# Performance work log

Hardware: AMD Instinct MI355X
Metric: run time of the kernel (lower is better)

Reference implementation:

```python
import jax, jax.numpy as jnp
import numpy as np
from jax import lax

EPS = 1e-08

def _sobel_edges(x, sx, sy):
    # x: [B, C, H, W]; depthwise 3x3 conv per channel, SAME padding.
    B, C, H, W = x.shape
    kx = jnp.tile(sx, (C, 1, 1, 1))  # [C,1,3,3] OIHW with feature_group_count=C
    ky = jnp.tile(sy, (C, 1, 1, 1))
    dn = ('NCHW', 'OIHW', 'NCHW')
    gx = lax.conv_general_dilated(x, kx, (1, 1), 'SAME',
                                  dimension_numbers=dn, feature_group_count=C)
    gy = lax.conv_general_dilated(x, ky, (1, 1), 'SAME',
                                  dimension_numbers=dn, feature_group_count=C)
    return jnp.sqrt(gx * gx + gy * gy + EPS)

def setup_inputs() -> dict:
    key = jax.random.key(0)
    k1, k2 = jax.random.split(key)
    B, C, H, W = 16, 8, 512, 512
    source_latent = jax.random.normal(k1, (B, C, H, W), dtype=jnp.float32)
    edited_latent = jax.random.normal(k2, (B, C, H, W), dtype=jnp.float32)
    sx = jnp.array([[-1., 0., 1.], [-2., 0., 2.], [-1., 0., 1.]], dtype=jnp.float32).reshape(1, 1, 3, 3)
    sy = jnp.array([[-1., -2., -1.], [0., 0., 0.], [1., 2., 1.]], dtype=jnp.float32).reshape(1, 1, 3, 3)
    return {"source_latent": source_latent, "edited_latent": edited_latent, "sx": sx, "sy": sy}

def reference(source_latent, edited_latent, sx, sy):
    e_src = _sobel_edges(source_latent, sx, sy)
    e_edit = _sobel_edges(edited_latent, sx, sy)
    diff = e_edit - e_src
    return jnp.mean(diff * diff)
```

## Files before the change

kernel.cpp:

```cpp
#include <hip/hip_runtime.h>


#define EPS 1e-8f

constexpr int W_DIM  = 512;
constexpr int H_DIM  = 512;
constexpr int NIMG   = 128;
constexpr int ROWS   = 16;
constexpr int CHUNKS = H_DIM / ROWS;
constexpr int TPB    = 128;
constexpr int NBLK   = NIMG * CHUNKS;
constexpr double TOTAL_ELEMS = 33554432.0;

__global__ __launch_bounds__(TPB) void edge_loss_stage1(
    const float* __restrict__ src, const float* __restrict__ edt,
    float* __restrict__ partial)
{
    const int blk   = blockIdx.x;
    const int n     = blk / CHUNKS;
    const int chunk = blk % CHUNKS;
    const int r0    = chunk * ROWS;
    const float* sbase = src + (size_t)n * H_DIM * W_DIM;
    const float* ebase = edt + (size_t)n * H_DIM * W_DIM;
    const int c0 = threadIdx.x * 4;

    float sa0[4], sa1[4], sa2[4], sb0[4], sb1[4], sb2[4];
    float ea0[4], ea1[4], ea2[4], eb0[4], eb1[4], eb2[4];

    auto loadrow = [&](const float* base, int h, float* a, float* b) {
        if (h < 0 || h >= H_DIM) {
            #pragma unroll
            for (int i = 0; i < 4; ++i) { a[i] = 0.f; b[i] = 0.f; }
            return;
        }
        const float* row = base + (size_t)h * W_DIM;
        float4 v = *reinterpret_cast<const float4*>(row + c0);
        float xl = (c0 > 0)          ? row[c0 - 1] : 0.f;
        float xr = (c0 + 4 < W_DIM)  ? row[c0 + 4] : 0.f;
        float p0 = xl,  p1 = v.x, p2 = v.y, p3 = v.z, p4 = v.w, p5 = xr;
        a[0] = p2 - p0;  b[0] = p0 + 2.f*p1 + p2;
        a[1] = p3 - p1;  b[1] = p1 + 2.f*p2 + p3;
        a[2] = p4 - p2;  b[2] = p2 + 2.f*p3 + p4;
        a[3] = p5 - p3;  b[3] = p3 + 2.f*p4 + p5;
    };

    loadrow(sbase, r0 - 1, sa0, sb0);
    loadrow(ebase, r0 - 1, ea0, eb0);
    loadrow(sbase, r0,     sa1, sb1);
    loadrow(ebase, r0,     ea1, eb1);

    float acc = 0.f;
    for (int h = r0; h < r0 + ROWS; ++h) {
        loadrow(sbase, h + 1, sa2, sb2);
        loadrow(ebase, h + 1, ea2, eb2);
        #pragma unroll
        for (int i = 0; i < 4; ++i) {
            float sgx = sa0[i] + 2.f*sa1[i] + sa2[i];
            float sgy = sb2[i] - sb0[i];
            float es  = __builtin_amdgcn_sqrtf(sgx*sgx + sgy*sgy + EPS);
            float egx = ea0[i] + 2.f*ea1[i] + ea2[i];
            float egy = eb2[i] - eb0[i];
            float ee  = __builtin_amdgcn_sqrtf(egx*egx + egy*egy + EPS);
            float d   = ee - es;
            acc += d * d;
        }
        #pragma unroll
        for (int i = 0; i < 4; ++i) {
            sa0[i] = sa1[i]; sa1[i] = sa2[i];
            sb0[i] = sb1[i]; sb1[i] = sb2[i];
            ea0[i] = ea1[i]; ea1[i] = ea2[i];
            eb0[i] = eb1[i]; eb1[i] = eb2[i];
        }
    }

    #pragma unroll
    for (int off = 32; off > 0; off >>= 1)
        acc += __shfl_down(acc, off);
    __shared__ float wsum[TPB / 64];
    const int wid  = threadIdx.x >> 6;
    const int lane = threadIdx.x & 63;
    if (lane == 0) wsum[wid] = acc;
    __syncthreads();
    if (threadIdx.x == 0) {
        float tot = 0.f;
        #pragma unroll
        for (int i = 0; i < TPB / 64; ++i) tot += wsum[i];
        partial[blk] = tot;
    }
}

__global__ __launch_bounds__(256) void edge_loss_stage2(
    const float* __restrict__ partial, float* __restrict__ out, int nparts)
{
    double acc = 0.0;
    for (int i = threadIdx.x; i < nparts; i += 256)
        acc += (double)partial[i];
    #pragma unroll
    for (int off = 32; off > 0; off >>= 1)
        acc += __shfl_down(acc, off);
    __shared__ double wsum[4];
    const int wid  = threadIdx.x >> 6;
    const int lane = threadIdx.x & 63;
    if (lane == 0) wsum[wid] = acc;
    __syncthreads();
    if (threadIdx.x == 0) {
        double t = 0.0;
        #pragma unroll
        for (int i = 0; i < 4; ++i) t += wsum[i];
        out[0] = (float)(t / TOTAL_ELEMS);
    }
}

extern "C" void kernel_launch(void* const* d_in, const int* in_sizes, int n_in,
                              void* d_out, int out_size, void* d_ws, size_t ws_size,
                              hipStream_t stream) {
    const float* src = (const float*)d_in[0];
    const float* edt = (const float*)d_in[1];
    float* out     = (float*)d_out;
    float* partial = (float*)d_ws;

    edge_loss_stage1<<<dim3(NBLK), dim3(TPB), 0, stream>>>(src, edt, partial);
    edge_loss_stage2<<<dim3(1), dim3(256), 0, stream>>>(partial, out, NBLK);
}
```

Before: 57.23 us.

## Use one wavefront per 512-wide row with 8 columns per lane and shuffled halos

Each wavefront now covers a full 512-wide row, with every lane holding 8 contiguous columns. Halo columns come from cross-lane shuffles rather than extra scalar global loads. Rows are double-buffered so the load for the next row is issued before the current row is consumed, and the vertical Sobel sums are carried as running partial accumulators. Blocks grow to 4 waves covering 64 rows each. This removes the redundant halo loads, raises the load width, and overlaps memory latency with compute, at the cost of more registers per thread.

New measurement: 123.1 us. +115.0%, slower.

```diff
diff --git a/kernel.cpp b/kernel.cpp
--- a/kernel.cpp
+++ b/kernel.cpp
@@ -3,88 +3,161 @@
 
 #define EPS 1e-8f
 
-constexpr int W_DIM  = 512;
-constexpr int H_DIM  = 512;
-constexpr int NIMG   = 128;
-constexpr int ROWS   = 16;
-constexpr int CHUNKS = H_DIM / ROWS;
-constexpr int TPB    = 128;
-constexpr int NBLK   = NIMG * CHUNKS;
+constexpr int W_DIM = 512;
+constexpr int H_DIM = 512;
+constexpr int NIMG  = 128;
+constexpr int ROWS  = 16;
+constexpr int WPB   = 4;
+constexpr int TPB   = 64 * WPB;
+constexpr int BLK_ROWS = ROWS * WPB;
+constexpr int BLKS_PER_IMG = H_DIM / BLK_ROWS;
+constexpr int NBLK  = NIMG * BLKS_PER_IMG;
 constexpr double TOTAL_ELEMS = 33554432.0;
 
-__global__ __launch_bounds__(TPB) void edge_loss_stage1(
+__global__ __launch_bounds__(TPB, 4) void edge_loss_stage1(
     const float* __restrict__ src, const float* __restrict__ edt,
     float* __restrict__ partial)
 {
-    const int blk   = blockIdx.x;
-    const int n     = blk / CHUNKS;
-    const int chunk = blk % CHUNKS;
-    const int r0    = chunk * ROWS;
-    const float* sbase = src + (size_t)n * H_DIM * W_DIM;
-    const float* ebase = edt + (size_t)n * H_DIM * W_DIM;
-    const int c0 = threadIdx.x * 4;
+    const int blk  = blockIdx.x;
+    const int img  = blk / BLKS_PER_IMG;
+    const int brow = (blk % BLKS_PER_IMG) * BLK_ROWS;
+    const int wid  = threadIdx.x >> 6;
+    const int lane = threadIdx.x & 63;
+    const int r0   = brow + wid * ROWS;
+    const int c0   = lane * 8;
 
-    float sa0[4], sa1[4], sa2[4], sb0[4], sb1[4], sb2[4];
-    float ea0[4], ea1[4], ea2[4], eb0[4], eb1[4], eb2[4];
+    const float* sbase = src + (size_t)img * (H_DIM * W_DIM) + c0;
+    const float* ebase = edt + (size_t)img * (H_DIM * W_DIM) + c0;
 
-    auto loadrow = [&](const float* base, int h, float* a, float* b) {
-        if (h < 0 || h >= H_DIM) {
-            #pragma unroll
-            for (int i = 0; i < 4; ++i) { a[i] = 0.f; b[i] = 0.f; }
-            return;
-        }
-        const float* row = base + (size_t)h * W_DIM;
-        float4 v = *reinterpret_cast<const float4*>(row + c0);
-        float xl = (c0 > 0)          ? row[c0 - 1] : 0.f;
-        float xr = (c0 + 4 < W_DIM)  ? row[c0 + 4] : 0.f;
-        float p0 = xl,  p1 = v.x, p2 = v.y, p3 = v.z, p4 = v.w, p5 = xr;
-        a[0] = p2 - p0;  b[0] = p0 + 2.f*p1 + p2;
-        a[1] = p3 - p1;  b[1] = p1 + 2.f*p2 + p3;
-        a[2] = p4 - p2;  b[2] = p2 + 2.f*p3 + p4;
-        a[3] = p5 - p3;  b[3] = p3 + 2.f*p4 + p5;
+    float sP0[8], sP1[8], sB0[8], sB1[8];
+    float eP0[8], eP1[8], eB0[8], eB1[8];
+    float spA[8], epA[8], spB[8], epB[8];
+    float acc = 0.f;
+
+    auto issue = [&](int h, float* sp, float* ep) {
+        int hc = h < 0 ? 0 : (h >= H_DIM ? H_DIM - 1 : h);
+        const float* srow = sbase + (size_t)hc * W_DIM;
+        const float* erow = ebase + (size_t)hc * W_DIM;
+        float4 s0 = reinterpret_cast<const float4*>(srow)[0];
+        float4 s1 = reinterpret_cast<const float4*>(srow)[1];
+        float4 e0 = reinterpret_cast<const float4*>(erow)[0];
+        float4 e1 = reinterpret_cast<const float4*>(erow)[1];
+        sp[0]=s0.x; sp[1]=s0.y; sp[2]=s0.z; sp[3]=s0.w;
+        sp[4]=s1.x; sp[5]=s1.y; sp[6]=s1.z; sp[7]=s1.w;
+        ep[0]=e0.x; ep[1]=e0.y; ep[2]=e0.z; ep[3]=e0.w;
+        ep[4]=e1.x; ep[5]=e1.y; ep[6]=e1.z; ep[7]=e1.w;
     };
 
-    loadrow(sbase, r0 - 1, sa0, sb0);
-    loadrow(ebase, r0 - 1, ea0, eb0);
-    loadrow(sbase, r0,     sa1, sb1);
-    loadrow(ebase, r0,     ea1, eb1);
+    auto consume = [&](const float* sp, const float* ep, int h) {
+        if (h < H_DIM) {
+            float spL = __shfl_up(sp[7], 1);  spL = lane ? spL : 0.f;
+            float spR = __shfl_down(sp[0], 1); spR = (lane == 63) ? 0.f : spR;
+            float epL = __shfl_up(ep[7], 1);  epL = lane ? epL : 0.f;
+            float epR = __shfl_down(ep[0], 1); epR = (lane == 63) ? 0.f : epR;
+            #pragma unroll
+            for (int i = 0; i < 8; ++i) {
+                float sm = (i == 0) ? spL : sp[i-1];
+                float sq = (i == 7) ? spR : sp[i+1];
+                float a  = sq - sm;
+                float b  = sm + 2.f*sp[i] + sq;
+                float gx = sP0[i] + a;
+                sP0[i] = fmaf(2.f, a, sP1[i]);
+                sP1[i] = a;
+                float gy = b - sB0[i];
+                sB0[i] = sB1[i]; sB1[i] = b;
+                float es = __builtin_amdgcn_sqrtf(fmaf(gx, gx, fmaf(gy, gy, EPS)));
 
-    float acc = 0.f;
-    for (int h = r0; h < r0 + ROWS; ++h) {
-        loadrow(sbase, h + 1, sa2, sb2);
-        loadrow(ebase, h + 1, ea2, eb2);
+                float em = (i == 0) ? epL : ep[i-1];
+                float eq = (i == 7) ? epR : ep[i+1];
+                float a2 = eq - em;
+                float b2 = em + 2.f*ep[i] + eq;
+                float gx2 = eP0[i] + a2;
+                eP0[i] = fmaf(2.f, a2, eP1[i]);
+                eP1[i] = a2;
+                float gy2 = b2 - eB0[i];
+                eB0[i] = eB1[i]; eB1[i] = b2;
+                float ee = __builtin_amdgcn_sqrtf(fmaf(gx2, gx2, fmaf(gy2, gy2, EPS)));
+
+                float d = ee - es;
+                acc = fmaf(d, d, acc);
+            }
+        } else {
+            #pragma unroll
+            for (int i = 0; i < 8; ++i) {
+                float gx = sP0[i];  sP0[i] = sP1[i]; sP1[i] = 0.f;
+                float gy = -sB0[i]; sB0[i] = sB1[i]; sB1[i] = 0.f;
+                float es = __builtin_amdgcn_sqrtf(fmaf(gx, gx, fmaf(gy, gy, EPS)));
+                float gx2 = eP0[i];  eP0[i] = eP1[i]; eP1[i] = 0.f;
+                float gy2 = -eB0[i]; eB0[i] = eB1[i]; eB1[i] = 0.f;
+                float ee = __builtin_amdgcn_sqrtf(fmaf(gx2, gx2, fmaf(gy2, gy2, EPS)));
+                float d = ee - es;
+                acc = fmaf(d, d, acc);
+            }
+        }
+    };
+
+    issue(r0 - 1, spA, epA);
+    issue(r0,     spB, epB);
+    if (r0 > 0) {
+        float spL = __shfl_up(spA[7], 1);  spL = lane ? spL : 0.f;
+        float spR = __shfl_down(spA[0], 1); spR = (lane == 63) ? 0.f : spR;
+        float epL = __shfl_up(epA[7], 1);  epL = lane ? epL : 0.f;
+        float epR = __shfl_down(epA[0], 1); epR = (lane == 63) ? 0.f : epR;
         #pragma unroll
-        for (int i = 0; i < 4; ++i) {
-            float sgx = sa0[i] + 2.f*sa1[i] + sa2[i];
-            float sgy = sb2[i] - sb0[i];
-            float es  = __builtin_amdgcn_sqrtf(sgx*sgx + sgy*sgy + EPS);
-            float egx = ea0[i] + 2.f*ea1[i] + ea2[i];
-            float egy = eb2[i] - eb0[i];
-            float ee  = __builtin_amdgcn_sqrtf(egx*egx + egy*egy + EPS);
-            float d   = ee - es;
-            acc += d * d;
+        for (int i = 0; i < 8; ++i) {
+            float sm = (i == 0) ? spL : spA[i-1];
+            float sq = (i == 7) ? spR : spA[i+1];
+            sP0[i] = sq - sm;
+            sB0[i] = sm + 2.f*spA[i] + sq;
+            float em = (i == 0) ? epL : epA[i-1];
+            float eq = (i == 7) ? epR : epA[i+1];
+            eP0[i] = eq - em;
+            eB0[i] = em + 2.f*epA[i] + eq;
         }
+    } else {
         #pragma unroll
-        for (int i = 0; i < 4; ++i) {
-            sa0[i] = sa1[i]; sa1[i] = sa2[i];
-            sb0[i] = sb1[i]; sb1[i] = sb2[i];
-            ea0[i] = ea1[i]; ea1[i] = ea2[i];
-            eb0[i] = eb1[i]; eb1[i] = eb2[i];
+        for (int i = 0; i < 8; ++i) { sP0[i]=0.f; sB0[i]=0.f; eP0[i]=0.f; eB0[i]=0.f; }
+    }
+    {
+        float spL = __shfl_up(spB[7], 1);  spL = lane ? spL : 0.f;
+        float spR = __shfl_down(spB[0], 1); spR = (lane == 63) ? 0.f : spR;
+        float epL = __shfl_up(epB[7], 1);  epL = lane ? epL : 0.f;
+        float epR = __shfl_down(epB[0], 1); epR = (lane == 63) ? 0.f : epR;
+        #pragma unroll
+        for (int i = 0; i < 8; ++i) {
+            float sm = (i == 0) ? spL : spB[i-1];
+            float sq = (i == 7) ? spR : spB[i+1];
+            float a  = sq - sm;
+            sP0[i] = fmaf(2.f, a, sP0[i]);
+            sP1[i] = a;
+            sB1[i] = sm + 2.f*spB[i] + sq;
+            float em = (i == 0) ? epL : epB[i-1];
+            float eq = (i == 7) ? epR : epB[i+1];
+            float a2 = eq - em;
+            eP0[i] = fmaf(2.f, a2, eP0[i]);
+            eP1[i] = a2;
+            eB1[i] = em + 2.f*epB[i] + eq;
         }
+    }
+    issue(r0 + 1, spA, epA);
+
+    for (int r = r0 + 1; r <= r0 + ROWS; r += 2) {
+        issue(r + 1, spB, epB);
+        consume(spA, epA, r);
+        if (r + 2 <= r0 + ROWS) issue(r + 2, spA, epA);
+        consume(spB, epB, r + 1);
     }
 
     #pragma unroll
     for (int off = 32; off > 0; off >>= 1)
         acc += __shfl_down(acc, off);
-    __shared__ float wsum[TPB / 64];
-    const int wid  = threadIdx.x >> 6;
-    const int lane = threadIdx.x & 63;
+    __shared__ float wsum[WPB];
     if (lane == 0) wsum[wid] = acc;
     __syncthreads();
     if (threadIdx.x == 0) {
         float tot = 0.f;
         #pragma unroll
-        for (int i = 0; i < TPB / 64; ++i) tot += wsum[i];
+        for (int i = 0; i < WPB; ++i) tot += wsum[i];
         partial[blk] = tot;
     }
 }
```
